# Optimization experiments

Hardware: AMD Instinct MI355X
Metric: run time of the kernel (lower is better)

The kernel has to match this reference:

```python
import jax, jax.numpy as jnp
import numpy as np

GAMMA = 0.96875
SCALE_BASE = 512.0


def _fixed_pos_embedding(scale):
    # scale: (L, d) where d = head_dim // 2
    L, d = scale.shape
    inv_freq = 1.0 / (10000.0 ** (jnp.arange(d, dtype=jnp.float32) / d))
    sinusoid = jnp.arange(L, dtype=jnp.float32)[:, None] * inv_freq  # (L, d)
    return jnp.sin(sinusoid), jnp.cos(sinusoid)


def _rotate_every_two(x):
    # (..., D) -> (..., D) with pairs (x0, x1) -> (-x1, x0)
    x1 = x[..., ::2]
    x2 = x[..., 1::2]
    return jnp.stack((-x2, x1), axis=-1).reshape(x.shape)


def _dup_interleave(m):
    # (L, d) -> (L, 2d), each column duplicated (matches rotary pairing)
    return jnp.repeat(m, 2, axis=-1)


def xpos(x, offset=0, downscale=False):
    # x: (B, S, D). Standard torchscale-style XPos rotary embedding.
    S, D = x.shape[-2], x.shape[-1]
    scale_vec = (jnp.arange(0, D, 2, dtype=jnp.float32) + 0.4 * D) / (1.4 * D)  # (D/2,)
    min_pos = -(S + offset) // 2
    max_pos = S + offset + min_pos
    power = jnp.arange(min_pos, max_pos, dtype=jnp.float32) / SCALE_BASE  # (S+offset,)
    scale = scale_vec ** power[:, None]  # (S+offset, D/2)
    sin, cos = _fixed_pos_embedding(scale)
    if scale.shape[0] > S:  # keep the last S positions
        scale, sin, cos = scale[-S:], sin[-S:], cos[-S:]
    if downscale:
        scale = 1.0 / scale
    sin = _dup_interleave(sin * scale)  # (S, D)
    cos = _dup_interleave(cos * scale)  # (S, D)
    return x * cos + _rotate_every_two(x) * sin


def _decay_mask(S, dtype):
    # D[n, m] = gamma^(n-m) if n >= m else 0  (lower triangular)
    m = jnp.arange(S)
    diff = m[:, None] - m  # (S, S)
    causal = diff >= 0
    exp = jnp.where(causal, diff, 0).astype(dtype)
    return jnp.where(causal, jnp.asarray(GAMMA, dtype) ** exp, jnp.zeros((), dtype))


def setup_inputs() -> dict:
    key = jax.random.key(0)
    kx, kq, kk, kv = jax.random.split(key, 4)
    B, S, H, Dh = 4, 4096, 2048, 256
    return {
        "x": jax.random.normal(kx, (B, S, H), dtype=jnp.float32),
        "w_q": jax.random.normal(kq, (H, Dh), dtype=jnp.float32),
        "w_k": jax.random.normal(kk, (H, Dh), dtype=jnp.float32),
        "w_v": jax.random.normal(kv, (H, Dh), dtype=jnp.float32),
    }


def reference(x, w_q, w_k, w_v):
    # x: (B, S, H) -> out: (B, S, Dh)
    B, S, _ = x.shape
    decay = _decay_mask(S, x.dtype)[None]  # (1, S, S)
    q = xpos(x @ w_q)                       # (B, S, Dh)
    k = xpos(x @ w_k, downscale=True)       # (B, S, Dh)
    v = x @ w_v                             # (B, S, Dh)
    ret = jnp.einsum("bsd,btd->bst", q, k) * decay  # (B, S, S)
    return jnp.einsum("bst,btd->bsd", ret, v)       # (B, S, Dh)
```

## Files before the change

kernel.cpp:

```cpp
#include <hip/hip_runtime.h>
#include <cstddef>
#include <cstdint>

#define Bn 4
#define Sn 4096
#define Hn 2048
#define Dn 256

typedef float f32x16 __attribute__((ext_vector_type(16)));
typedef short bf16x8 __attribute__((ext_vector_type(8)));

#define AS3 __attribute__((address_space(3)))
#define AS1 __attribute__((address_space(1)))

#define L2G -0.045803689613125f
#define GC 2.9526131e-4f

__device__ __forceinline__ unsigned short f2bf(float f) {
  union { float f; unsigned int u; } a; a.f = f;
  unsigned int r = a.u + 0x7fffu + ((a.u >> 16) & 1u);
  return (unsigned short)(r >> 16);
}
__device__ __forceinline__ float bf2f(unsigned int b) {
  union { unsigned int u; float f; } a; a.u = b << 16;
  return a.f;
}

__global__ __launch_bounds__(256) void rt_build(float* __restrict__ rt) {
  const int g = blockIdx.x * 256 + threadIdx.x;
  const int s = g >> 7;
  const int jp = g & 127;
  const float invf = exp2f((float)jp * (-13.287712379549449f / 128.0f));
  float sn, cs;
  sincosf((float)s * invf, &sn, &cs);
  const float l2sv = log2f((2.0f * jp + 102.4f) * (1.0f / 358.4f));
  const float pw = ((float)s - 2048.0f) * (1.0f / 512.0f);
  const float tl = (float)(s & 255) * L2G;
  const float ex = pw * l2sv + tl;
  const float eq = exp2f(ex), ek = exp2f(-ex);
  float2* q = (float2*)rt;
  float2* k = (float2*)(rt + 4096 * 256);
  q[(size_t)s * 128 + jp] = make_float2(cs * eq, sn * eq);
  k[(size_t)s * 128 + jp] = make_float2(cs * ek, sn * ek);
}

__global__ __launch_bounds__(256) void xbf_kernel(const float* __restrict__ x,
                                                  unsigned short* __restrict__ xb) {
  const size_t g = (size_t)blockIdx.x * 256 + threadIdx.x;
  const float* src = x + g * 16;
  unsigned short* dst = xb + g * 16;
  uint4 o0, o1;
  {
    float4 v0 = ((const float4*)src)[0];
    float4 v1 = ((const float4*)src)[1];
    float4 v2 = ((const float4*)src)[2];
    float4 v3 = ((const float4*)src)[3];
    o0.x = f2bf(v0.x) | ((unsigned int)f2bf(v0.y) << 16);
    o0.y = f2bf(v0.z) | ((unsigned int)f2bf(v0.w) << 16);
    o0.z = f2bf(v1.x) | ((unsigned int)f2bf(v1.y) << 16);
    o0.w = f2bf(v1.z) | ((unsigned int)f2bf(v1.w) << 16);
    o1.x = f2bf(v2.x) | ((unsigned int)f2bf(v2.y) << 16);
    o1.y = f2bf(v2.z) | ((unsigned int)f2bf(v2.w) << 16);
    o1.z = f2bf(v3.x) | ((unsigned int)f2bf(v3.y) << 16);
    o1.w = f2bf(v3.z) | ((unsigned int)f2bf(v3.w) << 16);
  }
  ((uint4*)dst)[0] = o0;
  ((uint4*)dst)[1] = o1;
}

__global__ __launch_bounds__(256) void wt_build(const float* __restrict__ wq,
                                                const float* __restrict__ wk,
                                                const float* __restrict__ wv,
                                                unsigned short* __restrict__ wt) {
  __shared__ __align__(16) unsigned short T[64][72];
  const int tid = threadIdx.x;
  const int k0 = blockIdx.x * 64;
  const int n0 = blockIdx.y * 64;
  const float* w = (n0 < 256) ? wq : (n0 < 512 ? wk : wv);
  const int nc0 = n0 & 255;
#pragma unroll
  for (int it = 0; it < 2; ++it) {
    int flat = it * 256 + tid;
    int r = flat >> 3, c8 = flat & 7;
    const float* src = w + (size_t)(k0 + r) * 256 + nc0 + c8 * 8;
    float4 v0 = *(const float4*)src;
    float4 v1 = *(const float4*)(src + 4);
    T[c8 * 8 + 0][r] = f2bf(v0.x); T[c8 * 8 + 1][r] = f2bf(v0.y);
    T[c8 * 8 + 2][r] = f2bf(v0.z); T[c8 * 8 + 3][r] = f2bf(v0.w);
    T[c8 * 8 + 4][r] = f2bf(v1.x); T[c8 * 8 + 5][r] = f2bf(v1.y);
    T[c8 * 8 + 6][r] = f2bf(v1.z); T[c8 * 8 + 7][r] = f2bf(v1.w);
  }
  __syncthreads();
#pragma unroll
  for (int it = 0; it < 2; ++it) {
    int flat = it * 256 + tid;
    int nr = flat >> 3, kc8 = flat & 7;
    int n = n0 + nr;
    int kc_sw = kc8 ^ (n & 7);
    uint4 val = *(const uint4*)&T[nr][kc8 * 8];
    *(uint4*)((char*)wt + (size_t)n * 4096 + (size_t)k0 * 2 + kc_sw * 16) = val;
  }
}

__global__ __launch_bounds__(256, 3) void proj2f_kernel(const unsigned short* __restrict__ xb,
                                                        const unsigned short* __restrict__ wt,
                                                        const float* __restrict__ rt,
                                                        unsigned short* __restrict__ qkv,
                                                        unsigned short* __restrict__ kt,
                                                        unsigned short* __restrict__ vt) {
  __shared__ __align__(16) char smem[32768];
  unsigned short* As = (unsigned short*)smem;
  unsigned short* Bs = (unsigned short*)(smem + 16384);
  const int tid = threadIdx.x;
  const int lane = tid & 63;
  const int wid = tid >> 6;
  const int wr = wid >> 1, wc = wid & 1;
  const int m0 = blockIdx.x * 128;
  const int n0 = blockIdx.y * 128;
  const int l31 = lane & 31, lh = lane >> 5;

  f32x16 acc[2][2];
#pragma unroll
  for (int i = 0; i < 2; ++i)
#pragma unroll
    for (int j = 0; j < 2; ++j) acc[i][j] = 0.0f;

  for (int k0 = 0; k0 < Hn; k0 += 64) {
    AS3 char* ldsa = (AS3 char*)As;
    AS3 char* ldsb = (AS3 char*)Bs;
#pragma unroll
    for (int i = 0; i < 4; ++i) {
      int ou = i * 4096 + wid * 1024;
      int o = ou + lane * 16;
      int row = o >> 7, colB = o & 127;
      const char* srcA = (const char*)xb + (size_t)(m0 + row) * 4096 + k0 * 2 + (colB ^ ((row & 7) << 4));
      __builtin_amdgcn_global_load_lds((const AS1 unsigned int*)srcA,
                                       (AS3 unsigned int*)(ldsa + ou), 16, 0, 0);
      const char* srcB = (const char*)wt + (size_t)(n0 + row) * 4096 + k0 * 2 + colB;
      __builtin_amdgcn_global_load_lds((const AS1 unsigned int*)srcB,
                                       (AS3 unsigned int*)(ldsb + ou), 16, 0, 0);
    }
    __syncthreads();
#pragma unroll
    for (int kc = 0; kc < 4; ++kc) {
      const int kb = kc * 32 + lh * 16;
      bf16x8 a[2], b[2];
#pragma unroll
      for (int i = 0; i < 2; ++i) {
        int mr = wr * 64 + i * 32 + l31;
        a[i] = *(const bf16x8*)((const char*)As + mr * 128 + (kb ^ ((mr & 7) << 4)));
        int nr = wc * 64 + i * 32 + l31;
        b[i] = *(const bf16x8*)((const char*)Bs + nr * 128 + (kb ^ ((nr & 7) << 4)));
      }
#pragma unroll
      for (int i = 0; i < 2; ++i)
#pragma unroll
        for (int j = 0; j < 2; ++j)
          acc[i][j] = __builtin_amdgcn_mfma_f32_32x32x16_bf16(a[i], b[j], acc[i][j], 0, 0, 0);
    }
    __syncthreads();
  }

  const int kind = n0 >> 8;
  const int n0q = n0 & 255;
  const int bidx = m0 >> 12;
  const int t0b = m0 & 4095;

  if (kind < 2) {
    const float* rtb = rt + (size_t)kind * (4096 * 256);
    const int jp0 = (n0q + wc * 64 + l31) >> 1;
    const int jp1 = (n0q + wc * 64 + 32 + l31) >> 1;
    const int odd = l31 & 1;
#pragma unroll
    for (int i = 0; i < 2; ++i)
#pragma unroll
      for (int reg = 0; reg < 16; ++reg) {
        const int mm = m0 + wr * 64 + i * 32 + (reg & 3) + 8 * (reg >> 2) + 4 * lh;
        const int s = mm & (Sn - 1);
#pragma unroll
        for (int j = 0; j < 2; ++j) {
          const int jp = j ? jp1 : jp0;
          const float2 cf = *(const float2*)(rtb + (size_t)s * 256 + jp * 2);
          float v = acc[i][j][reg];
          float p = __shfl_xor(v, 1, 64);
          acc[i][j][reg] = odd ? (v * cf.x + p * cf.y) : (v * cf.x - p * cf.y);
        }
      }
  }

  if (kind == 0) {
#pragma unroll
    for (int i = 0; i < 2; ++i)
#pragma unroll
      for (int j = 0; j < 2; ++j)
#pragma unroll
        for (int reg = 0; reg < 16; ++reg) {
          int m = m0 + wr * 64 + i * 32 + (reg & 3) + 8 * (reg >> 2) + 4 * lh;
          int n = n0q + wc * 64 + j * 32 + l31;
          qkv[(size_t)m * 768 + n] = f2bf(acc[i][j][reg]);
        }
  } else {
    if (kind == 1) {
#pragma unroll
      for (int i = 0; i < 2; ++i)
#pragma unroll
        for (int j = 0; j < 2; ++j)
#pragma unroll
          for (int reg = 0; reg < 16; ++reg) {
            int m = m0 + wr * 64 + i * 32 + (reg & 3) + 8 * (reg >> 2) + 4 * lh;
            int d = n0q + wc * 64 + j * 32 + l31;
            qkv[(size_t)m * 768 + 256 + (d ^ ((m & 7) << 3))] = f2bf(acc[i][j][reg]);
          }
    }
#pragma unroll
    for (int i = 0; i < 2; ++i)
#pragma unroll
      for (int j = 0; j < 2; ++j) {
        const int dl = wc * 64 + j * 32 + l31;
#pragma unroll
        for (int k8 = 0; k8 < 8; ++k8) {
          const int r0 = 2 * k8;
          const int t = wr * 64 + i * 32 + (r0 & 3) + 8 * (r0 >> 2) + 4 * lh;
          unsigned int pk;
          asm("v_cvt_pk_bf16_f32 %0, %1, %2" : "=v"(pk)
              : "v"(acc[i][j][r0]), "v"(acc[i][j][r0 + 1]));
          *(unsigned int*)(smem + dl * 256 + ((2 * t) ^ ((dl & 7) << 4))) = pk;
        }
      }
    __syncthreads();
    unsigned short* dst = (kind == 1) ? kt : vt;
#pragma unroll
    for (int p = 0; p < 8; ++p) {
      const int fl = p * 256 + tid;
      const int dl = fl >> 4, t8 = fl & 15;
      uint4 val = *(const uint4*)(smem + dl * 256 + ((t8 * 16) ^ ((dl & 7) << 4)));
      *(uint4*)(dst + (size_t)(bidx * 256 + n0q + dl) * 4096 + t0b + t8 * 8) = val;
    }
  }
}

__global__ __launch_bounds__(256, 2) void proj_kernel(const float* __restrict__ x,
                                                      const unsigned short* __restrict__ wt,
                                                      unsigned short* __restrict__ qkv) {
  __shared__ __align__(16) unsigned short As[128 * 64];
  __shared__ __align__(16) unsigned short Bs[128 * 64];
  const int tid = threadIdx.x;
  const int lane = tid & 63;
  const int wid = tid >> 6;
  const int wr = wid >> 1, wc = wid & 1;
  const int m0 = blockIdx.x * 128;
  const int n0 = blockIdx.y * 128;
  const int l31 = lane & 31, lh = lane >> 5;

  f32x16 acc[2][2];
#pragma unroll
  for (int i = 0; i < 2; ++i)
#pragma unroll
    for (int j = 0; j < 2; ++j) acc[i][j] = 0.0f;

  for (int k0 = 0; k0 < Hn; k0 += 64) {
    {
      AS3 char* ldsb = (AS3 char*)Bs;
#pragma unroll
      for (int i = 0; i < 4; ++i) {
        int ou = i * 4096 + wid * 1024;
        int o = ou + lane * 16;
        int row = o >> 7, col = o & 127;
        const char* src = (const char*)wt + (size_t)(n0 + row) * 4096 + k0 * 2 + col;
        __builtin_amdgcn_global_load_lds((const AS1 unsigned int*)src,
                                         (AS3 unsigned int*)(ldsb + ou), 16, 0, 0);
      }
    }
#pragma unroll
    for (int i = 0; i < 4; ++i) {
      int o = i * 256 + tid;
      int row = o >> 3, c8 = o & 7;
      const float* src = x + (size_t)(m0 + row) * 2048 + k0 + c8 * 8;
      float4 v0 = *(const float4*)src;
      float4 v1 = *(const float4*)(src + 4);
      uint4 val;
      val.x = f2bf(v0.x) | ((unsigned int)f2bf(v0.y) << 16);
      val.y = f2bf(v0.z) | ((unsigned int)f2bf(v0.w) << 16);
      val.z = f2bf(v1.x) | ((unsigned int)f2bf(v1.y) << 16);
      val.w = f2bf(v1.z) | ((unsigned int)f2bf(v1.w) << 16);
      *(uint4*)((char*)As + row * 128 + ((c8 * 16) ^ ((row & 7) << 4))) = val;
    }
    __syncthreads();
#pragma unroll
    for (int kc = 0; kc < 4; ++kc) {
      const int kb = kc * 32 + lh * 16;
      bf16x8 a[2], b[2];
#pragma unroll
      for (int i = 0; i < 2; ++i) {
        int mr = wr * 64 + i * 32 + l31;
        a[i] = *(const bf16x8*)((const char*)As + mr * 128 + (kb ^ ((mr & 7) << 4)));
        int nr = wc * 64 + i * 32 + l31;
        b[i] = *(const bf16x8*)((const char*)Bs + nr * 128 + (kb ^ ((nr & 7) << 4)));
      }
#pragma unroll
      for (int i = 0; i < 2; ++i)
#pragma unroll
        for (int j = 0; j < 2; ++j)
          acc[i][j] = __builtin_amdgcn_mfma_f32_32x32x16_bf16(a[i], b[j], acc[i][j], 0, 0, 0);
    }
    __syncthreads();
  }
  const bool khalf = (n0 >= 256 && n0 < 512);
#pragma unroll
  for (int i = 0; i < 2; ++i)
#pragma unroll
    for (int j = 0; j < 2; ++j)
#pragma unroll
      for (int reg = 0; reg < 16; ++reg) {
        int m = m0 + wr * 64 + i * 32 + (reg & 3) + 8 * (reg >> 2) + 4 * lh;
        int n = n0 + wc * 64 + j * 32 + l31;
        if (khalf) n = 256 + ((n - 256) ^ ((m & 7) << 3));
        qkv[(size_t)m * 768 + n] = f2bf(acc[i][j][reg]);
      }
}

__global__ __launch_bounds__(256) void xpos_kernel(unsigned short* __restrict__ qkv) {
  const int g = blockIdx.x * 256 + threadIdx.x;
  const int m = g >> 5;
  const int c = g & 31;
  const float s = (float)(m & (Sn - 1));
  unsigned short* qrow = qkv + (size_t)m * 768;
  const int csw = c ^ (m & 7);
  uint4 qv = *(uint4*)(qrow + c * 8);
  uint4 kv = *(uint4*)(qrow + 256 + csw * 8);
  unsigned int* qu = (unsigned int*)&qv;
  unsigned int* ku = (unsigned int*)&kv;
  const float pw = (s - 2048.0f) * (1.0f / 512.0f);
  const float gp = exp2f((float)(m & 255) * L2G);
#pragma unroll
  for (int p = 0; p < 4; ++p) {
    const int jp = c * 4 + p;
    const float invf = exp2f((float)jp * (-13.287712379549449f / 128.0f));
    float sn, cs;
    sincosf(s * invf, &sn, &cs);
    const float sv = (2.0f * jp + 102.4f) * (1.0f / 358.4f);
    const float scq = exp2f(pw * log2f(sv)) * gp;
    const float sci = 1.0f / scq;
    float q0 = bf2f(qu[p] & 0xffffu), q1 = bf2f(qu[p] >> 16);
    float k0 = bf2f(ku[p] & 0xffffu), k1 = bf2f(ku[p] >> 16);
    float q0r = (q0 * cs - q1 * sn) * scq;
    float q1r = (q1 * cs + q0 * sn) * scq;
    float k0r = (k0 * cs - k1 * sn) * sci;
    float k1r = (k1 * cs + k0 * sn) * sci;
    qu[p] = f2bf(q0r) | ((unsigned int)f2bf(q1r) << 16);
    ku[p] = f2bf(k0r) | ((unsigned int)f2bf(k1r) << 16);
  }
  *(uint4*)(qrow + c * 8) = qv;
  *(uint4*)(qrow + 256 + csw * 8) = kv;
}

__global__ __launch_bounds__(256) void kvt_build(const unsigned short* __restrict__ qkv,
                                                 unsigned short* __restrict__ kt,
                                                 unsigned short* __restrict__ vt) {
  __shared__ __align__(16) unsigned short Tk[64][72];
  __shared__ __align__(16) unsigned short Tv[64][72];
  const int tid = threadIdx.x;
  const int t0 = blockIdx.x * 64;
  const int d0 = blockIdx.y * 64;
  const int b = blockIdx.z;
  const size_t rowb = ((size_t)b * Sn + t0) * 1536;
#pragma unroll
  for (int it = 0; it < 2; ++it) {
    int flat = it * 256 + tid;
    int r = flat >> 3, c8 = flat & 7;
    int kc = (d0 >> 3) + c8;
    int kcs = kc ^ (r & 7);
    uint4 kvv = *(const uint4*)((const char*)qkv + rowb + (size_t)r * 1536 + 512 + kcs * 16);
    uint4 vvv = *(const uint4*)((const char*)qkv + rowb + (size_t)r * 1536 + 1024 + (size_t)(d0 + c8 * 8) * 2);
    const unsigned short* ke = (const unsigned short*)&kvv;
    const unsigned short* ve = (const unsigned short*)&vvv;
#pragma unroll
    for (int e = 0; e < 8; ++e) { Tk[c8 * 8 + e][r] = ke[e]; Tv[c8 * 8 + e][r] = ve[e]; }
  }
  __syncthreads();
#pragma unroll
  for (int it = 0; it < 2; ++it) {
    int flat = it * 256 + tid;
    int dr = flat >> 3, tc8 = flat & 7;
    *(uint4*)(kt + (size_t)(b * 256 + d0 + dr) * 4096 + t0 + tc8 * 8) = *(const uint4*)&Tk[dr][tc8 * 8];
    *(uint4*)(vt + (size_t)(b * 256 + d0 + dr) * 4096 + t0 + tc8 * 8) = *(const uint4*)&Tv[dr][tc8 * 8];
  }
}

__global__ __launch_bounds__(256) void mbuild_kernel(const unsigned short* __restrict__ kt,
                                                     const unsigned short* __restrict__ vt,
                                                     unsigned short* __restrict__ mt) {
  const int tid = threadIdx.x;
  const int lane = tid & 63;
  const int wid = tid >> 6;
  const int l31 = lane & 31, lh = lane >> 5;
  const int jc = blockIdx.x;
  const int quad = blockIdx.y;
  const int b = blockIdx.z;
  const int d2w = ((quad >> 1) * 2 + (wid >> 1)) * 64;
  const int d1w = ((quad & 1) * 2 + (wid & 1)) * 64;
  const size_t tb = (size_t)jc * 256;

  f32x16 acc[2][2];
#pragma unroll
  for (int i = 0; i < 2; ++i)
#pragma unroll
    for (int j = 0; j < 2; ++j) acc[i][j] = 0.0f;

#pragma unroll 2
  for (int dc = 0; dc < 16; ++dc) {
    const int ko = dc * 32 + lh * 16;
    bf16x8 a[2], bb[2];
#pragma unroll
    for (int i = 0; i < 2; ++i) {
      a[i]  = *(const bf16x8*)((const char*)vt + ((size_t)(b * 256 + d2w + i * 32 + l31) * 4096 + tb) * 2 + ko);
      bb[i] = *(const bf16x8*)((const char*)kt + ((size_t)(b * 256 + d1w + i * 32 + l31) * 4096 + tb) * 2 + ko);
    }
#pragma unroll
    for (int i = 0; i < 2; ++i)
#pragma unroll
      for (int j = 0; j < 2; ++j)
        acc[i][j] = __builtin_amdgcn_mfma_f32_32x32x16_bf16(a[i], bb[j], acc[i][j], 0, 0, 0);
  }
  unsigned short* dst = mt + ((size_t)(b * 16 + jc) << 16);
#pragma unroll
  for (int i = 0; i < 2; ++i)
#pragma unroll
    for (int j = 0; j < 2; ++j)
#pragma unroll
      for (int reg = 0; reg < 16; ++reg) {
        int row = d2w + i * 32 + (reg & 3) + 8 * (reg >> 2) + 4 * lh;
        int col = d1w + j * 32 + l31;
        dst[row * 256 + col] = f2bf(acc[i][j][reg]);
      }
}

__global__ __launch_bounds__(256) void scan_kernel(unsigned short* __restrict__ mt) {
  const int e0 = (blockIdx.x * 256 + threadIdx.x) * 4;
  const int b = blockIdx.y;
  unsigned short* base = mt + ((size_t)b << 20);
  float s0 = 0.f, s1 = 0.f, s2 = 0.f, s3 = 0.f;
  for (int j = 1; j < 16; ++j) {
    unsigned short* p = base + ((size_t)(j - 1) << 16) + e0;
    uint2 mv = *(const uint2*)p;
    s0 = GC * (s0 + bf2f(mv.x & 0xffffu));
    s1 = GC * (s1 + bf2f(mv.x >> 16));
    s2 = GC * (s2 + bf2f(mv.y & 0xffffu));
    s3 = GC * (s3 + bf2f(mv.y >> 16));
    uint2 w;
    w.x = f2bf(s0) | ((unsigned int)f2bf(s1) << 16);
    w.y = f2bf(s2) | ((unsigned int)f2bf(s3) << 16);
    *(uint2*)p = w;
  }
}

__global__ __launch_bounds__(256, 2) void retc_kernel(const unsigned short* __restrict__ qkv,
                                                      const unsigned short* __restrict__ vt,
                                                      const unsigned short* __restrict__ mt,
                                                      float* __restrict__ out) {
  __shared__ float cmb[2][32][128];
  const int tid = threadIdx.x;
  const int lane = tid & 63;
  const int tw = tid >> 6;
  const int l31 = lane & 31, lh = lane >> 5;
  const int st = blockIdx.x;
  const int dh = blockIdx.y;
  const int b = blockIdx.z;
  const int j = st >> 3;
  const int base = st & ~7;
  const int s0 = st * 32;
  const int d0 = dh * 128;

  bf16x8 qf[16];
  {
    const char* qrow = (const char*)qkv + ((size_t)b * Sn + s0 + l31) * 1536;
#pragma unroll
    for (int dc = 0; dc < 16; ++dc)
      qf[dc] = *(const bf16x8*)(qrow + dc * 32 + lh * 16);
  }

  f32x16 acc[4];
#pragma unroll
  for (int i = 0; i < 4; ++i) acc[i] = 0.0f;

  if (j > 0) {
    const char* Sj = (const char*)mt + ((size_t)(b * 16 + j - 1) << 17);
#pragma unroll
    for (int dcl = 0; dcl < 4; ++dcl) {
      const int dc = tw * 4 + dcl;
#pragma unroll
      for (int g = 0; g < 4; ++g) {
        const int d2 = d0 + g * 32 + l31;
        bf16x8 sbf = *(const bf16x8*)(Sj + (size_t)d2 * 512 + dc * 32 + lh * 16);
        acc[g] = __builtin_amdgcn_mfma_f32_32x32x16_bf16(qf[dc], sbf, acc[g], 0, 0, 0);
      }
    }
  }

  const int sg = s0 + l31;
  const int ksw = (l31 & 7) << 4;
  for (int tt = base; tt <= st; ++tt) {
    if (((tt - base) & 3) != tw) continue;
    const bool msk = (tt == st);
    const int t0 = tt * 32;

    f32x16 sacc = 0.0f;
    const char* krow = (const char*)qkv + ((size_t)b * Sn + t0 + l31) * 1536 + 512;
    __builtin_amdgcn_s_setprio(1);
#pragma unroll
    for (int dc = 0; dc < 16; ++dc) {
      bf16x8 kf = *(const bf16x8*)(krow + ((dc * 32 + lh * 16) ^ ksw));
      sacc = __builtin_amdgcn_mfma_f32_32x32x16_bf16(kf, qf[dc], sacc, 0, 0, 0);
    }
    __builtin_amdgcn_s_setprio(0);

    unsigned int P[8];
#pragma unroll
    for (int k = 0; k < 8; ++k) {
      const int r0 = 2 * k;
      float f0 = sacc[r0], f1 = sacc[r0 + 1];
      if (msk) {
        const int tg0 = t0 + (r0 & 3) + 8 * (r0 >> 2) + 4 * lh;
        f0 = (sg - tg0 >= 0) ? f0 : 0.0f;
        f1 = (sg - tg0 - 1 >= 0) ? f1 : 0.0f;
      }
      unsigned int pk;
      asm("v_cvt_pk_bf16_f32 %0, %1, %2" : "=v"(pk) : "v"(f0), "v"(f1));
      P[k] = pk;
    }
    asm volatile("v_permlane32_swap_b32 %0, %1" : "+v"(P[0]), "+v"(P[2]));
    asm volatile("v_permlane32_swap_b32 %0, %1" : "+v"(P[1]), "+v"(P[3]));
    asm volatile("v_permlane32_swap_b32 %0, %1" : "+v"(P[4]), "+v"(P[6]));
    asm volatile("v_permlane32_swap_b32 %0, %1" : "+v"(P[5]), "+v"(P[7]));

    __builtin_amdgcn_s_setprio(1);
#pragma unroll
    for (int kc = 0; kc < 2; ++kc) {
      uint4 pw;
      pw.x = P[kc * 4 + 0]; pw.y = P[kc * 4 + 1];
      pw.z = P[kc * 4 + 2]; pw.w = P[kc * 4 + 3];
      bf16x8 pf = *(const bf16x8*)&pw;
#pragma unroll
      for (int g = 0; g < 4; ++g) {
        const int d = d0 + g * 32 + l31;
        bf16x8 vf = *(const bf16x8*)((const char*)vt +
            ((size_t)(b * 256 + d) * 4096 + t0) * 2 + kc * 32 + lh * 16);
        acc[g] = __builtin_amdgcn_mfma_f32_32x32x16_bf16(pf, vf, acc[g], 0, 0, 0);
      }
    }
    __builtin_amdgcn_s_setprio(0);
  }

  if (tw >= 2) {
#pragma unroll
    for (int g = 0; g < 4; ++g)
#pragma unroll
      for (int reg = 0; reg < 16; ++reg) {
        int sl = (reg & 3) + 8 * (reg >> 2) + 4 * lh;
        cmb[tw - 2][sl][g * 32 + l31] = acc[g][reg];
      }
  }
  __syncthreads();
  if (tw < 2) {
#pragma unroll
    for (int g = 0; g < 4; ++g)
#pragma unroll
      for (int reg = 0; reg < 16; ++reg) {
        int sl = (reg & 3) + 8 * (reg >> 2) + 4 * lh;
        acc[g][reg] += cmb[tw][sl][g * 32 + l31];
      }
  }
  __syncthreads();
  if (tw == 1) {
#pragma unroll
    for (int g = 0; g < 4; ++g)
#pragma unroll
      for (int reg = 0; reg < 16; ++reg) {
        int sl = (reg & 3) + 8 * (reg >> 2) + 4 * lh;
        cmb[0][sl][g * 32 + l31] = acc[g][reg];
      }
  }
  __syncthreads();
  if (tw == 0) {
#pragma unroll
    for (int g = 0; g < 4; ++g)
#pragma unroll
      for (int reg = 0; reg < 16; ++reg) {
        int sl = (reg & 3) + 8 * (reg >> 2) + 4 * lh;
        int c = g * 32 + l31;
        out[((size_t)(b * Sn + s0 + sl)) * 256 + d0 + c] = acc[g][reg] + cmb[0][sl][c];
      }
  }
}

extern "C" void kernel_launch(void* const* d_in, const int* in_sizes, int n_in,
                              void* d_out, int out_size, void* d_ws, size_t ws_size,
                              hipStream_t stream) {
  (void)in_sizes; (void)n_in; (void)out_size;
  const float* x  = (const float*)d_in[0];
  const float* wq = (const float*)d_in[1];
  const float* wk = (const float*)d_in[2];
  const float* wv = (const float*)d_in[3];
  float* out = (float*)d_out;
  char* ws = (char*)d_ws;

  unsigned short* qkv = (unsigned short*)(ws);
  unsigned short* vt  = (unsigned short*)(ws + 25165824);
  unsigned short* kt  = (unsigned short*)(ws + 33554432);
  unsigned short* mt  = (unsigned short*)(ws + 41943040);

  const size_t NEED_BIG = 128974848;
  if (ws_size >= NEED_BIG) {
    unsigned short* xb = (unsigned short*)(ws + 50331648);
    unsigned short* wt = (unsigned short*)(ws + 117440512);
    float*          rtab = (float*)(ws + 120586240);
    rt_build<<<2048, 256, 0, stream>>>(rtab);
    xbf_kernel<<<8192, 256, 0, stream>>>(x, xb);
    wt_build<<<dim3(32, 12), 256, 0, stream>>>(wq, wk, wv, wt);
    proj2f_kernel<<<dim3(128, 6), 256, 0, stream>>>(xb, wt, rtab, qkv, kt, vt);
  } else {
    unsigned short* wt = (unsigned short*)(ws + 41943040);
    wt_build<<<dim3(32, 12), 256, 0, stream>>>(wq, wk, wv, wt);
    proj_kernel<<<dim3(128, 6), 256, 0, stream>>>(x, wt, qkv);
    xpos_kernel<<<2048, 256, 0, stream>>>(qkv);
    kvt_build<<<dim3(64, 4, 4), 256, 0, stream>>>(qkv, kt, vt);
  }
  mbuild_kernel<<<dim3(16, 4, 4), 256, 0, stream>>>(kt, vt, mt);
  scan_kernel<<<dim3(64, 4), 256, 0, stream>>>(mt);
  retc_kernel<<<dim3(128, 2, 4), 256, 0, stream>>>(qkv, vt, mt, out);
}
```

Measured before the change: 180.6 us.

## Fuse prep kernels, widen projection N-tile to 256, split retention output dims

Merges the rotary-table, x-to-bf16 and weight-transpose kernels into one launch indexed by block ID, cutting launch overhead. The projection GEMM now computes a full 256-wide output slice per block (128x256 tile, 48KB LDS, 2 blocks/SM), which halves the re-reads of x and lets each block handle a whole q/k/v kind. The K/V transpose epilogue runs in two halves to fit in LDS. The retention kernel now splits the output dimension into four 64-wide pieces instead of two 128-wide ones. That doubles the grid and lowers register pressure, but the Q loads and decay work are repeated across more blocks.

```diff
diff --git a/kernel.cpp b/kernel.cpp
--- a/kernel.cpp
+++ b/kernel.cpp
@@ -26,31 +26,37 @@
   return a.f;
 }
 
-__global__ __launch_bounds__(256) void rt_build(float* __restrict__ rt) {
-  const int g = blockIdx.x * 256 + threadIdx.x;
-  const int s = g >> 7;
-  const int jp = g & 127;
-  const float invf = exp2f((float)jp * (-13.287712379549449f / 128.0f));
-  float sn, cs;
-  sincosf((float)s * invf, &sn, &cs);
-  const float l2sv = log2f((2.0f * jp + 102.4f) * (1.0f / 358.4f));
-  const float pw = ((float)s - 2048.0f) * (1.0f / 512.0f);
-  const float tl = (float)(s & 255) * L2G;
-  const float ex = pw * l2sv + tl;
-  const float eq = exp2f(ex), ek = exp2f(-ex);
-  float2* q = (float2*)rt;
-  float2* k = (float2*)(rt + 4096 * 256);
-  q[(size_t)s * 128 + jp] = make_float2(cs * eq, sn * eq);
-  k[(size_t)s * 128 + jp] = make_float2(cs * ek, sn * ek);
-}
-
-__global__ __launch_bounds__(256) void xbf_kernel(const float* __restrict__ x,
-                                                  unsigned short* __restrict__ xb) {
-  const size_t g = (size_t)blockIdx.x * 256 + threadIdx.x;
-  const float* src = x + g * 16;
-  unsigned short* dst = xb + g * 16;
-  uint4 o0, o1;
-  {
+__global__ __launch_bounds__(256) void prep_kernel(const float* __restrict__ x,
+                                                   const float* __restrict__ wq,
+                                                   const float* __restrict__ wk,
+                                                   const float* __restrict__ wv,
+                                                   unsigned short* __restrict__ xb,
+                                                   unsigned short* __restrict__ wt,
+                                                   float* __restrict__ rt) {
+  __shared__ __align__(16) unsigned short T[64][72];
+  const int bx = blockIdx.x;
+  const int tid = threadIdx.x;
+  if (bx < 2048) {
+    const int g = bx * 256 + tid;
+    const int s = g >> 7;
+    const int jp = g & 127;
+    const float invf = exp2f((float)jp * (-13.287712379549449f / 128.0f));
+    float sn, cs;
+    sincosf((float)s * invf, &sn, &cs);
+    const float l2sv = log2f((2.0f * jp + 102.4f) * (1.0f / 358.4f));
+    const float pw = ((float)s - 2048.0f) * (1.0f / 512.0f);
+    const float tl = (float)(s & 255) * L2G;
+    const float ex = pw * l2sv + tl;
+    const float eq = exp2f(ex), ek = exp2f(-ex);
+    float2* q = (float2*)rt;
+    float2* k = (float2*)(rt + 4096 * 256);
+    q[(size_t)s * 128 + jp] = make_float2(cs * eq, sn * eq);
+    k[(size_t)s * 128 + jp] = make_float2(cs * ek, sn * ek);
+  } else if (bx < 10240) {
+    const size_t g = (size_t)(bx - 2048) * 256 + tid;
+    const float* src = x + g * 16;
+    unsigned short* dst = xb + g * 16;
+    uint4 o0, o1;
     float4 v0 = ((const float4*)src)[0];
     float4 v1 = ((const float4*)src)[1];
     float4 v2 = ((const float4*)src)[2];
@@ -63,9 +69,187 @@
     o1.y = f2bf(v2.z) | ((unsigned int)f2bf(v2.w) << 16);
     o1.z = f2bf(v3.x) | ((unsigned int)f2bf(v3.y) << 16);
     o1.w = f2bf(v3.z) | ((unsigned int)f2bf(v3.w) << 16);
-  }
-  ((uint4*)dst)[0] = o0;
-  ((uint4*)dst)[1] = o1;
+    ((uint4*)dst)[0] = o0;
+    ((uint4*)dst)[1] = o1;
+  } else {
+    const int bw = bx - 10240;
+    const int k0 = (bw & 31) * 64;
+    const int n0 = (bw >> 5) * 64;
+    const float* w = (n0 < 256) ? wq : (n0 < 512 ? wk : wv);
+    const int nc0 = n0 & 255;
+#pragma unroll
+    for (int it = 0; it < 2; ++it) {
+      int flat = it * 256 + tid;
+      int r = flat >> 3, c8 = flat & 7;
+      const float* src = w + (size_t)(k0 + r) * 256 + nc0 + c8 * 8;
+      float4 v0 = *(const float4*)src;
+      float4 v1 = *(const float4*)(src + 4);
+      T[c8 * 8 + 0][r] = f2bf(v0.x); T[c8 * 8 + 1][r] = f2bf(v0.y);
+      T[c8 * 8 + 2][r] = f2bf(v0.z); T[c8 * 8 + 3][r] = f2bf(v0.w);
+      T[c8 * 8 + 4][r] = f2bf(v1.x); T[c8 * 8 + 5][r] = f2bf(v1.y);
+      T[c8 * 8 + 6][r] = f2bf(v1.z); T[c8 * 8 + 7][r] = f2bf(v1.w);
+    }
+    __syncthreads();
+#pragma unroll
+    for (int it = 0; it < 2; ++it) {
+      int flat = it * 256 + tid;
+      int nr = flat >> 3, kc8 = flat & 7;
+      int n = n0 + nr;
+      int kc_sw = kc8 ^ (n & 7);
+      uint4 val = *(const uint4*)&T[nr][kc8 * 8];
+      *(uint4*)((char*)wt + (size_t)n * 4096 + (size_t)k0 * 2 + kc_sw * 16) = val;
+    }
+  }
+}
+
+__global__ __launch_bounds__(256, 2) void proj3_kernel(const unsigned short* __restrict__ xb,
+                                                       const unsigned short* __restrict__ wt,
+                                                       const float* __restrict__ rt,
+                                                       unsigned short* __restrict__ qkv,
+                                                       unsigned short* __restrict__ kt,
+                                                       unsigned short* __restrict__ vt) {
+  __shared__ __align__(16) char smem[49152];
+  unsigned short* As = (unsigned short*)smem;
+  unsigned short* Bs = (unsigned short*)(smem + 16384);
+  const int tid = threadIdx.x;
+  const int lane = tid & 63;
+  const int wid = tid >> 6;
+  const int wr = wid >> 1, wc = wid & 1;
+  const int m0 = blockIdx.x * 128;
+  const int kind = blockIdx.y;
+  const int l31 = lane & 31, lh = lane >> 5;
+
+  f32x16 acc[2][4];
+#pragma unroll
+  for (int i = 0; i < 2; ++i)
+#pragma unroll
+    for (int j = 0; j < 4; ++j) acc[i][j] = 0.0f;
+
+  for (int k0 = 0; k0 < Hn; k0 += 64) {
+    AS3 char* ldsa = (AS3 char*)As;
+    AS3 char* ldsb = (AS3 char*)Bs;
+#pragma unroll
+    for (int i = 0; i < 4; ++i) {
+      int ou = i * 4096 + wid * 1024;
+      int o = ou + lane * 16;
+      int row = o >> 7, colB = o & 127;
+      const char* srcA = (const char*)xb + (size_t)(m0 + row) * 4096 + k0 * 2 + (colB ^ ((row & 7) << 4));
+      __builtin_amdgcn_global_load_lds((const AS1 unsigned int*)srcA,
+                                       (AS3 unsigned int*)(ldsa + ou), 16, 0, 0);
+    }
+#pragma unroll
+    for (int i = 0; i < 8; ++i) {
+      int ou = i * 4096 + wid * 1024;
+      int o = ou + lane * 16;
+      int row = o >> 7, colB = o & 127;
+      const char* srcB = (const char*)wt + (size_t)(kind * 256 + row) * 4096 + k0 * 2 + colB;
+      __builtin_amdgcn_global_load_lds((const AS1 unsigned int*)srcB,
+                                       (AS3 unsigned int*)(ldsb + ou), 16, 0, 0);
+    }
+    __syncthreads();
+#pragma unroll
+    for (int kc = 0; kc < 4; ++kc) {
+      const int kb = kc * 32 + lh * 16;
+      bf16x8 a[2], b[4];
+#pragma unroll
+      for (int i = 0; i < 2; ++i) {
+        int mr = wr * 64 + i * 32 + l31;
+        a[i] = *(const bf16x8*)((const char*)As + mr * 128 + (kb ^ ((mr & 7) << 4)));
+      }
+#pragma unroll
+      for (int j = 0; j < 4; ++j) {
+        int nr = wc * 128 + j * 32 + l31;
+        b[j] = *(const bf16x8*)((const char*)Bs + nr * 128 + (kb ^ ((nr & 7) << 4)));
+      }
+#pragma unroll
+      for (int i = 0; i < 2; ++i)
+#pragma unroll
+        for (int j = 0; j < 4; ++j)
+          acc[i][j] = __builtin_amdgcn_mfma_f32_32x32x16_bf16(a[i], b[j], acc[i][j], 0, 0, 0);
+    }
+    __syncthreads();
+  }
+
+  const int bidx = m0 >> 12;
+  const int t0b = m0 & 4095;
+
+  if (kind < 2) {
+    const float* rtb = rt + (size_t)kind * (4096 * 256);
+    int jp[4];
+#pragma unroll
+    for (int j = 0; j < 4; ++j) jp[j] = (wc * 128 + j * 32 + l31) >> 1;
+    const int odd = l31 & 1;
+#pragma unroll
+    for (int i = 0; i < 2; ++i)
+#pragma unroll
+      for (int reg = 0; reg < 16; ++reg) {
+        const int mm = m0 + wr * 64 + i * 32 + (reg & 3) + 8 * (reg >> 2) + 4 * lh;
+        const int s = mm & (Sn - 1);
+#pragma unroll
+        for (int j = 0; j < 4; ++j) {
+          const float2 cf = *(const float2*)(rtb + (size_t)s * 256 + jp[j] * 2);
+          float v = acc[i][j][reg];
+          float p = __shfl_xor(v, 1, 64);
+          acc[i][j][reg] = odd ? (v * cf.x + p * cf.y) : (v * cf.x - p * cf.y);
+        }
+      }
+  }
+
+  if (kind == 0) {
+#pragma unroll
+    for (int i = 0; i < 2; ++i)
+#pragma unroll
+      for (int j = 0; j < 4; ++j)
+#pragma unroll
+        for (int reg = 0; reg < 16; ++reg) {
+          int m = m0 + wr * 64 + i * 32 + (reg & 3) + 8 * (reg >> 2) + 4 * lh;
+          int n = wc * 128 + j * 32 + l31;
+          qkv[(size_t)m * 768 + n] = f2bf(acc[i][j][reg]);
+        }
+  } else {
+    if (kind == 1) {
+#pragma unroll
+      for (int i = 0; i < 2; ++i)
+#pragma unroll
+        for (int j = 0; j < 4; ++j)
+#pragma unroll
+          for (int reg = 0; reg < 16; ++reg) {
+            int m = m0 + wr * 64 + i * 32 + (reg & 3) + 8 * (reg >> 2) + 4 * lh;
+            int d = wc * 128 + j * 32 + l31;
+            qkv[(size_t)m * 768 + 256 + (d ^ ((m & 7) << 3))] = f2bf(acc[i][j][reg]);
+          }
+    }
+    unsigned short* dst = (kind == 1) ? kt : vt;
+#pragma unroll
+    for (int h = 0; h < 2; ++h) {
+      __syncthreads();
+      if (wc == h) {
+#pragma unroll
+        for (int i = 0; i < 2; ++i)
+#pragma unroll
+          for (int j = 0; j < 4; ++j) {
+            const int dl = j * 32 + l31;
+#pragma unroll
+            for (int k8 = 0; k8 < 8; ++k8) {
+              const int r0 = 2 * k8;
+              const int t = wr * 64 + i * 32 + (r0 & 3) + 8 * (r0 >> 2) + 4 * lh;
+              unsigned int pk;
+              asm("v_cvt_pk_bf16_f32 %0, %1, %2" : "=v"(pk)
+                  : "v"(acc[i][j][r0]), "v"(acc[i][j][r0 + 1]));
+              *(unsigned int*)(smem + dl * 256 + ((2 * t) ^ ((dl & 7) << 4))) = pk;
+            }
+          }
+      }
+      __syncthreads();
+#pragma unroll
+      for (int p = 0; p < 8; ++p) {
+        const int fl = p * 256 + tid;
+        const int dl = fl >> 4, t8 = fl & 15;
+        uint4 val = *(const uint4*)(smem + dl * 256 + ((t8 * 16) ^ ((dl & 7) << 4)));
+        *(uint4*)(dst + (size_t)(bidx * 256 + h * 128 + dl) * 4096 + t0b + t8 * 8) = val;
+      }
+    }
+  }
 }
 
 __global__ __launch_bounds__(256) void wt_build(const float* __restrict__ wq,
@@ -99,143 +283,6 @@
     int kc_sw = kc8 ^ (n & 7);
     uint4 val = *(const uint4*)&T[nr][kc8 * 8];
     *(uint4*)((char*)wt + (size_t)n * 4096 + (size_t)k0 * 2 + kc_sw * 16) = val;
-  }
-}
-
-__global__ __launch_bounds__(256, 3) void proj2f_kernel(const unsigned short* __restrict__ xb,
-                                                        const unsigned short* __restrict__ wt,
-                                                        const float* __restrict__ rt,
-                                                        unsigned short* __restrict__ qkv,
-                                                        unsigned short* __restrict__ kt,
-                                                        unsigned short* __restrict__ vt) {
-  __shared__ __align__(16) char smem[32768];
-  unsigned short* As = (unsigned short*)smem;
-  unsigned short* Bs = (unsigned short*)(smem + 16384);
-  const int tid = threadIdx.x;
-  const int lane = tid & 63;
-  const int wid = tid >> 6;
-  const int wr = wid >> 1, wc = wid & 1;
-  const int m0 = blockIdx.x * 128;
-  const int n0 = blockIdx.y * 128;
-  const int l31 = lane & 31, lh = lane >> 5;
-
-  f32x16 acc[2][2];
-#pragma unroll
-  for (int i = 0; i < 2; ++i)
-#pragma unroll
-    for (int j = 0; j < 2; ++j) acc[i][j] = 0.0f;
-
-  for (int k0 = 0; k0 < Hn; k0 += 64) {
-    AS3 char* ldsa = (AS3 char*)As;
-    AS3 char* ldsb = (AS3 char*)Bs;
-#pragma unroll
-    for (int i = 0; i < 4; ++i) {
-      int ou = i * 4096 + wid * 1024;
-      int o = ou + lane * 16;
-      int row = o >> 7, colB = o & 127;
-      const char* srcA = (const char*)xb + (size_t)(m0 + row) * 4096 + k0 * 2 + (colB ^ ((row & 7) << 4));
-      __builtin_amdgcn_global_load_lds((const AS1 unsigned int*)srcA,
-                                       (AS3 unsigned int*)(ldsa + ou), 16, 0, 0);
-      const char* srcB = (const char*)wt + (size_t)(n0 + row) * 4096 + k0 * 2 + colB;
-      __builtin_amdgcn_global_load_lds((const AS1 unsigned int*)srcB,
-                                       (AS3 unsigned int*)(ldsb + ou), 16, 0, 0);
-    }
-    __syncthreads();
-#pragma unroll
-    for (int kc = 0; kc < 4; ++kc) {
-      const int kb = kc * 32 + lh * 16;
-      bf16x8 a[2], b[2];
-#pragma unroll
-      for (int i = 0; i < 2; ++i) {
-        int mr = wr * 64 + i * 32 + l31;
-        a[i] = *(const bf16x8*)((const char*)As + mr * 128 + (kb ^ ((mr & 7) << 4)));
-        int nr = wc * 64 + i * 32 + l31;
-        b[i] = *(const bf16x8*)((const char*)Bs + nr * 128 + (kb ^ ((nr & 7) << 4)));
-      }
-#pragma unroll
-      for (int i = 0; i < 2; ++i)
-#pragma unroll
-        for (int j = 0; j < 2; ++j)
-          acc[i][j] = __builtin_amdgcn_mfma_f32_32x32x16_bf16(a[i], b[j], acc[i][j], 0, 0, 0);
-    }
-    __syncthreads();
-  }
-
-  const int kind = n0 >> 8;
-  const int n0q = n0 & 255;
-  const int bidx = m0 >> 12;
-  const int t0b = m0 & 4095;
-
-  if (kind < 2) {
-    const float* rtb = rt + (size_t)kind * (4096 * 256);
-    const int jp0 = (n0q + wc * 64 + l31) >> 1;
-    const int jp1 = (n0q + wc * 64 + 32 + l31) >> 1;
-    const int odd = l31 & 1;
-#pragma unroll
-    for (int i = 0; i < 2; ++i)
-#pragma unroll
-      for (int reg = 0; reg < 16; ++reg) {
-        const int mm = m0 + wr * 64 + i * 32 + (reg & 3) + 8 * (reg >> 2) + 4 * lh;
-        const int s = mm & (Sn - 1);
-#pragma unroll
-        for (int j = 0; j < 2; ++j) {
-          const int jp = j ? jp1 : jp0;
-          const float2 cf = *(const float2*)(rtb + (size_t)s * 256 + jp * 2);
-          float v = acc[i][j][reg];
-          float p = __shfl_xor(v, 1, 64);
-          acc[i][j][reg] = odd ? (v * cf.x + p * cf.y) : (v * cf.x - p * cf.y);
-        }
-      }
-  }
-
-  if (kind == 0) {
-#pragma unroll
-    for (int i = 0; i < 2; ++i)
-#pragma unroll
-      for (int j = 0; j < 2; ++j)
-#pragma unroll
-        for (int reg = 0; reg < 16; ++reg) {
-          int m = m0 + wr * 64 + i * 32 + (reg & 3) + 8 * (reg >> 2) + 4 * lh;
-          int n = n0q + wc * 64 + j * 32 + l31;
-          qkv[(size_t)m * 768 + n] = f2bf(acc[i][j][reg]);
-        }
-  } else {
-    if (kind == 1) {
-#pragma unroll
-      for (int i = 0; i < 2; ++i)
-#pragma unroll
-        for (int j = 0; j < 2; ++j)
-#pragma unroll
-          for (int reg = 0; reg < 16; ++reg) {
-            int m = m0 + wr * 64 + i * 32 + (reg & 3) + 8 * (reg >> 2) + 4 * lh;
-            int d = n0q + wc * 64 + j * 32 + l31;
-            qkv[(size_t)m * 768 + 256 + (d ^ ((m & 7) << 3))] = f2bf(acc[i][j][reg]);
-          }
-    }
-#pragma unroll
-    for (int i = 0; i < 2; ++i)
-#pragma unroll
-      for (int j = 0; j < 2; ++j) {
-        const int dl = wc * 64 + j * 32 + l31;
-#pragma unroll
-        for (int k8 = 0; k8 < 8; ++k8) {
-          const int r0 = 2 * k8;
-          const int t = wr * 64 + i * 32 + (r0 & 3) + 8 * (r0 >> 2) + 4 * lh;
-          unsigned int pk;
-          asm("v_cvt_pk_bf16_f32 %0, %1, %2" : "=v"(pk)
-              : "v"(acc[i][j][r0]), "v"(acc[i][j][r0 + 1]));
-          *(unsigned int*)(smem + dl * 256 + ((2 * t) ^ ((dl & 7) << 4))) = pk;
-        }
-      }
-    __syncthreads();
-    unsigned short* dst = (kind == 1) ? kt : vt;
-#pragma unroll
-    for (int p = 0; p < 8; ++p) {
-      const int fl = p * 256 + tid;
-      const int dl = fl >> 4, t8 = fl & 15;
-      uint4 val = *(const uint4*)(smem + dl * 256 + ((t8 * 16) ^ ((dl & 7) << 4)));
-      *(uint4*)(dst + (size_t)(bidx * 256 + n0q + dl) * 4096 + t0b + t8 * 8) = val;
-    }
   }
 }
 
@@ -458,7 +505,7 @@
                                                       const unsigned short* __restrict__ vt,
                                                       const unsigned short* __restrict__ mt,
                                                       float* __restrict__ out) {
-  __shared__ float cmb[2][32][128];
+  __shared__ float cmb[2][32][64];
   const int tid = threadIdx.x;
   const int lane = tid & 63;
   const int tw = tid >> 6;
@@ -469,7 +516,7 @@
   const int j = st >> 3;
   const int base = st & ~7;
   const int s0 = st * 32;
-  const int d0 = dh * 128;
+  const int d0 = dh * 64;
 
   bf16x8 qf[16];
   {
@@ -479,9 +526,9 @@
       qf[dc] = *(const bf16x8*)(qrow + dc * 32 + lh * 16);
   }
 
-  f32x16 acc[4];
-#pragma unroll
-  for (int i = 0; i < 4; ++i) acc[i] = 0.0f;
+  f32x16 acc[2];
+#pragma unroll
+  for (int i = 0; i < 2; ++i) acc[i] = 0.0f;
 
   if (j > 0) {
     const char* Sj = (const char*)mt + ((size_t)(b * 16 + j - 1) << 17);
@@ -489,7 +536,7 @@
     for (int dcl = 0; dcl < 4; ++dcl) {
       const int dc = tw * 4 + dcl;
 #pragma unroll
-      for (int g = 0; g < 4; ++g) {
+      for (int g = 0; g < 2; ++g) {
         const int d2 = d0 + g * 32 + l31;
         bf16x8 sbf = *(const bf16x8*)(Sj + (size_t)d2 * 512 + dc * 32 + lh * 16);
         acc[g] = __builtin_amdgcn_mfma_f32_32x32x16_bf16(qf[dc], sbf, acc[g], 0, 0, 0);
@@ -541,7 +588,7 @@
       pw.z = P[kc * 4 + 2]; pw.w = P[kc * 4 + 3];
       bf16x8 pf = *(const bf16x8*)&pw;
 #pragma unroll
-      for (int g = 0; g < 4; ++g) {
+      for (int g = 0; g < 2; ++g) {
         const int d = d0 + g * 32 + l31;
         bf16x8 vf = *(const bf16x8*)((const char*)vt +
             ((size_t)(b * 256 + d) * 4096 + t0) * 2 + kc * 32 + lh * 16);
@@ -553,7 +600,7 @@
 
   if (tw >= 2) {
 #pragma unroll
-    for (int g = 0; g < 4; ++g)
+    for (int g = 0; g < 2; ++g)
 #pragma unroll
       for (int reg = 0; reg < 16; ++reg) {
         int sl = (reg & 3) + 8 * (reg >> 2) + 4 * lh;
@@ -563,7 +610,7 @@
   __syncthreads();
   if (tw < 2) {
 #pragma unroll
-    for (int g = 0; g < 4; ++g)
+    for (int g = 0; g < 2; ++g)
 #pragma unroll
       for (int reg = 0; reg < 16; ++reg) {
         int sl = (reg & 3) + 8 * (reg >> 2) + 4 * lh;
@@ -573,7 +620,7 @@
   __syncthreads();
   if (tw == 1) {
 #pragma unroll
-    for (int g = 0; g < 4; ++g)
+    for (int g = 0; g < 2; ++g)
 #pragma unroll
       for (int reg = 0; reg < 16; ++reg) {
         int sl = (reg & 3) + 8 * (reg >> 2) + 4 * lh;
@@ -583,7 +630,7 @@
   __syncthreads();
   if (tw == 0) {
 #pragma unroll
-    for (int g = 0; g < 4; ++g)
+    for (int g = 0; g < 2; ++g)
 #pragma unroll
       for (int reg = 0; reg < 16; ++reg) {
         int sl = (reg & 3) + 8 * (reg >> 2) + 4 * lh;
@@ -614,10 +661,8 @@
     unsigned short* xb = (unsigned short*)(ws + 50331648);
     unsigned short* wt = (unsigned short*)(ws + 117440512);
     float*          rtab = (float*)(ws + 120586240);
-    rt_build<<<2048, 256, 0, stream>>>(rtab);
-    xbf_kernel<<<8192, 256, 0, stream>>>(x, xb);
-    wt_build<<<dim3(32, 12), 256, 0, stream>>>(wq, wk, wv, wt);
-    proj2f_kernel<<<dim3(128, 6), 256, 0, stream>>>(xb, wt, rtab, qkv, kt, vt);
+    prep_kernel<<<10624, 256, 0, stream>>>(x, wq, wk, wv, xb, wt, rtab);
+    proj3_kernel<<<dim3(128, 3), 256, 0, stream>>>(xb, wt, rtab, qkv, kt, vt);
   } else {
     unsigned short* wt = (unsigned short*)(ws + 41943040);
     wt_build<<<dim3(32, 12), 256, 0, stream>>>(wq, wk, wv, wt);
@@ -627,5 +672,5 @@
   }
   mbuild_kernel<<<dim3(16, 4, 4), 256, 0, stream>>>(kt, vt, mt);
   scan_kernel<<<dim3(64, 4), 256, 0, stream>>>(mt);
-  retc_kernel<<<dim3(128, 2, 4), 256, 0, stream>>>(qkv, vt, mt, out);
-}
+  retc_kernel<<<dim3(128, 4, 4), 256, 0, stream>>>(qkv, vt, mt, out);
+}
```

Result: slower. 204.8 us (+13.4%).
